# Kernel tuning notes

Measured on AMD Instinct MI355X. Metric: run time of the kernel, lower is better.

## Reference

```python
import jax, jax.numpy as jnp
import numpy as np

K = 8                   # num_RQS_bins
MIN_BW = 1e-6; MIN_BH = 1e-6; MIN_D = 1e-6
TAIL = 12.0             # tail_bound for 'linear' tails
# binary masks for num_inputs=4: kept (conditioning) dims and transformed dims per layer
MASK_IDX = [(0, 2), (1, 3), (0, 1), (2, 3)]
INV_IDX = [(1, 3), (0, 2), (2, 3), (0, 1)]


def _rqs_forward(x, uw, uh, ud):
    """Unconstrained rational-quadratic spline, forward (direct) pass.
    x: [B,F]; uw,uh: [B,F,K]; ud: [B,F,K-1]. Returns (y, logabsdet) each [B,F]."""
    const = float(np.log(np.exp(1.0 - MIN_D) - 1.0))
    ud = jnp.pad(ud, ((0, 0), (0, 0), (1, 1)), constant_values=const)  # [B,F,K+1]
    inside = (x >= -TAIL) & (x <= TAIL)
    xc = jnp.clip(x, -TAIL, TAIL)

    widths = MIN_BW + (1.0 - MIN_BW * K) * jax.nn.softmax(uw, -1)
    cumw = jnp.pad(jnp.cumsum(widths, -1), ((0, 0), (0, 0), (1, 0)))
    cumw = 2.0 * TAIL * cumw - TAIL
    cumw = cumw.at[..., 0].set(-TAIL).at[..., -1].set(TAIL)
    widths = cumw[..., 1:] - cumw[..., :-1]

    heights = MIN_BH + (1.0 - MIN_BH * K) * jax.nn.softmax(uh, -1)
    cumh = jnp.pad(jnp.cumsum(heights, -1), ((0, 0), (0, 0), (1, 0)))
    cumh = 2.0 * TAIL * cumh - TAIL
    cumh = cumh.at[..., 0].set(-TAIL).at[..., -1].set(TAIL)
    heights = cumh[..., 1:] - cumh[..., :-1]

    derivs = MIN_D + jax.nn.softplus(ud)  # [B,F,K+1]

    # searchsorted over bin edges (forward mode uses cumwidths)
    idx = jnp.clip(jnp.sum((xc[..., None] >= cumw).astype(jnp.int32), -1) - 1, 0, K - 1)
    g = lambda t: jnp.take_along_axis(t, idx[..., None], axis=-1)[..., 0]
    in_cw, in_w = g(cumw), g(widths)
    in_ch, in_h = g(cumh), g(heights)
    delta = in_h / in_w
    d_k, d_k1 = g(derivs), g(derivs[..., 1:])

    theta = (xc - in_cw) / in_w
    tomt = theta * (1.0 - theta)
    num = in_h * (delta * theta ** 2 + d_k * tomt)
    den = delta + (d_k + d_k1 - 2.0 * delta) * tomt
    y = in_ch + num / den
    dnum = delta ** 2 * (d_k1 * theta ** 2 + 2.0 * delta * tomt + d_k * (1.0 - theta) ** 2)
    lad = jnp.log(dnum) - 2.0 * jnp.log(den)

    return jnp.where(inside, y, x), jnp.where(inside, lad, 0.0)


def setup_inputs() -> dict:
    key = jax.random.key(0)
    ks = jax.random.split(key, 5)
    B, H = 262144, 128
    OM = 3 * K - 1  # 23 params per transformed dim
    inputs = jax.random.normal(ks[0], (B, 4), jnp.float32)
    cond_inputs = jax.random.uniform(ks[1], (B, 1), jnp.float32)
    W1 = jax.random.normal(ks[2], (4, H, 3), jnp.float32) / np.sqrt(3.0)
    b1 = jnp.zeros((4, H), jnp.float32)
    W2 = jax.random.normal(ks[3], (4, H, H), jnp.float32) / np.sqrt(float(H))
    b2 = jnp.zeros((4, H), jnp.float32)
    W3 = jax.random.normal(ks[4], (4, 2 * OM, H), jnp.float32) / np.sqrt(float(H))
    b3 = jnp.zeros((4, 2 * OM), jnp.float32)
    return {"inputs": inputs, "cond_inputs": cond_inputs,
            "W1": W1, "b1": b1, "W2": W2, "b2": b2, "W3": W3, "b3": b3}


def reference(inputs, cond_inputs, W1, b1, W2, b2, W3, b3):
    B = inputs.shape[0]
    x = inputs
    logdets = jnp.zeros((B, 1), dtype=inputs.dtype)
    for l in range(4):  # fixed small number of coupling layers
        midx = list(MASK_IDX[l]); iidx = list(INV_IDX[l])
        m_in = jnp.concatenate([x[:, midx], cond_inputs], -1)  # [B,3]
        h = jax.nn.relu(m_in @ W1[l].T + b1[l])
        h = jax.nn.relu(h @ W2[l].T + b2[l])
        params = h @ W3[l].T + b3[l]  # [B, F*(3K-1)]
        F = len(iidx)
        tp = jnp.swapaxes(params.reshape(B, 3 * K - 1, F), 1, 2)  # [B,F,3K-1]
        y, lad = _rqs_forward(x[:, iidx], tp[..., :K], tp[..., K:2 * K], tp[..., 2 * K:])
        x = x.at[:, iidx].set(y)
        logdets = logdets + jnp.sum(lad, -1, keepdims=True)
    return x, logdets
```

## Files before the change

kernel.cpp:

```cpp
#include <hip/hip_runtime.h>

#define TAILB 12.0f
#define INV2048 4.8828125e-4f

typedef _Float16 half8 __attribute__((ext_vector_type(8)));
typedef _Float16 half4 __attribute__((ext_vector_type(4)));
typedef __fp16 fp16x2 __attribute__((ext_vector_type(2)));
typedef __attribute__((ext_vector_type(4))) float f32x4;

#define MFMAH __builtin_amdgcn_mfma_f32_16x16x32_f16

#define WAVE_SYNC() do {                                  \
    __builtin_amdgcn_sched_barrier(0);                    \
    asm volatile("s_waitcnt lgkmcnt(0)" ::: "memory");    \
    __builtin_amdgcn_sched_barrier(0);                    \
} while (0)

__device__ __forceinline__ float softplus_f(float z) {
    return (z > 15.f) ? z : __logf(1.f + __expf(z));
}

__device__ __forceinline__ void split2h(float v, _Float16& o0, _Float16& o1) {
    _Float16 h0 = (_Float16)v;
    float r1 = v - (float)h0;
    o0 = h0;
    o1 = (_Float16)(r1 * 2048.0f);
}

__device__ __forceinline__ void split4_pk(const float* v, half4& p0, half4& p1) {
    fp16x2 lo = __builtin_amdgcn_cvt_pkrtz(v[0], v[1]);
    fp16x2 hi = __builtin_amdgcn_cvt_pkrtz(v[2], v[3]);
    float r0 = (v[0] - (float)lo.x) * 2048.f;
    float r1 = (v[1] - (float)lo.y) * 2048.f;
    float r2 = (v[2] - (float)hi.x) * 2048.f;
    float r3 = (v[3] - (float)hi.y) * 2048.f;
    fp16x2 rlo = __builtin_amdgcn_cvt_pkrtz(r0, r1);
    fp16x2 rhi = __builtin_amdgcn_cvt_pkrtz(r2, r3);
    p0 = (half4){(_Float16)lo.x, (_Float16)lo.y, (_Float16)hi.x, (_Float16)hi.y};
    p1 = (half4){(_Float16)rlo.x, (_Float16)rlo.y, (_Float16)rhi.x, (_Float16)rhi.y};
}

__global__ __launch_bounds__(256)
void prep_v16(const float* __restrict__ W1, const float* __restrict__ b1,
              const float* __restrict__ W2, const float* __restrict__ W3,
              _Float16* __restrict__ W2F, _Float16* __restrict__ W3F,
              float4* __restrict__ w1p)
{
    int id = blockIdx.x * 256 + threadIdx.x;
    if (id < 65536) {
        int j = id & 7, ln = (id >> 3) & 63, tile = id >> 9;
        int cs = tile & 3, t = (tile >> 2) & 1, wv = (tile >> 3) & 3, l = tile >> 5;
        int n = 32 * wv + 16 * t + (ln & 15);
        int k = 32 * cs + 8 * (ln >> 4) + j;
        _Float16 a, b;
        split2h(W2[l * 16384 + n * 128 + k], a, b);
        W2F[(tile * 2 + 0) * 512 + ln * 8 + j] = a;
        W2F[(tile * 2 + 1) * 512 + ln * 8 + j] = b;
    } else if (id < 90112) {
        int t2 = id - 65536;
        int j = t2 & 7, ln = (t2 >> 3) & 63, tile3 = t2 >> 9;
        int cs = tile3 & 3, q = tile3 >> 2;
        int wv = q % 3, l = q / 3;
        int p = 16 * wv + (ln & 15);
        int n = 32 * cs + 8 * (ln >> 4) + j;
        float v = (p < 46) ? W3[l * 5888 + p * 128 + n] : 0.f;
        _Float16 a, b;
        split2h(v, a, b);
        W3F[(tile3 * 2 + 0) * 512 + ln * 8 + j] = a;
        W3F[(tile3 * 2 + 1) * 512 + ln * 8 + j] = b;
    } else if (id < 90624) {
        int t = id - 90112;
        int l = t >> 7, k = t & 127;
        float4 v;
        v.x = W1[l * 384 + k * 3 + 0];
        v.y = W1[l * 384 + k * 3 + 1];
        v.z = W1[l * 384 + k * 3 + 2];
        v.w = b1[l * 128 + k];
        w1p[t] = v;
    }
}

__global__ __launch_bounds__(64, 3)
void rqs_v16(const float* __restrict__ inp, const float* __restrict__ cond,
             const _Float16* __restrict__ W2F, const _Float16* __restrict__ W3F,
             const float4* __restrict__ w1p,
             const float* __restrict__ b2, const float* __restrict__ b3,
             float* __restrict__ out, int B)
{
    __shared__ __align__(16) char P[8192];
    __shared__ float xbuf[32][5];

    char* plw = P;
    const char* pl = P;

    const int ln   = threadIdx.x;
    const int base = blockIdx.x * 32;
    const int sm   = ln & 15;
    const int qd   = ln >> 4;
    const int s1   = ln & 31;
    const int hi   = ln >> 5;

    int rdK[2][2];
    #pragma unroll
    for (int st = 0; st < 2; ++st)
        #pragma unroll
        for (int csl = 0; csl < 2; ++csl) {
            int row = 16 * st + sm;
            rdK[st][csl] = row * 128 + (((4 * csl + qd) ^ (row & 7)) << 4);
        }

    if (ln < 32) {
        float4 xi = reinterpret_cast<const float4*>(inp)[base + ln];
        xbuf[ln][0] = xi.x; xbuf[ln][1] = xi.y;
        xbuf[ln][2] = xi.z; xbuf[ln][3] = xi.w;
        xbuf[ln][4] = cond[base + ln];
    }
    float ladreg = 0.f;
    WAVE_SYNC();

    #pragma unroll 1
    for (int l = 0; l < 4; ++l) {
        int mi0, mi1, ii0, ii1;
        switch (l) {
            case 0:  mi0 = 0; mi1 = 2; ii0 = 1; ii1 = 3; break;
            case 1:  mi0 = 1; mi1 = 3; ii0 = 0; ii1 = 2; break;
            case 2:  mi0 = 0; mi1 = 1; ii0 = 2; ii1 = 3; break;
            default: mi0 = 2; mi1 = 3; ii0 = 0; ii1 = 1; break;
        }

        half8 bf[2][4][2];
        {
            float m0 = xbuf[s1][mi0], m1 = xbuf[s1][mi1], cc = xbuf[s1][4];
            const float4* w1l = w1p + l * 128;
            #pragma unroll
            for (int kh = 0; kh < 2; ++kh) {
                #pragma unroll
                for (int j4 = 0; j4 < 4; ++j4) {
                    int gl = 4 * hi + j4;
                    int g  = 8 * kh + gl;
                    float v[8];
                    #pragma unroll
                    for (int r = 0; r < 8; ++r) {
                        float4 w4 = w1l[g * 8 + r];
                        v[r] = fmaxf(fmaf(w4.x, m0, fmaf(w4.y, m1, fmaf(w4.z, cc, w4.w))), 0.f);
                    }
                    half4 a0, a1, b0h, b1h;
                    split4_pk(v, a0, a1);
                    split4_pk(v + 4, b0h, b1h);
                    half8 p0 = {a0.x, a0.y, a0.z, a0.w, b0h.x, b0h.y, b0h.z, b0h.w};
                    half8 p1 = {a1.x, a1.y, a1.z, a1.w, b1h.x, b1h.y, b1h.z, b1h.w};
                    char* wp = plw + s1 * 128 + ((gl ^ (s1 & 7)) << 4);
                    *(half8*)(wp)        = p0;
                    *(half8*)(wp + 4096) = p1;
                }
                WAVE_SYNC();
                #pragma unroll
                for (int st = 0; st < 2; ++st)
                    #pragma unroll
                    for (int csl = 0; csl < 2; ++csl) {
                        bf[st][2 * kh + csl][0] = *(const half8*)(pl + rdK[st][csl]);
                        bf[st][2 * kh + csl][1] = *(const half8*)(pl + rdK[st][csl] + 4096);
                    }
                WAVE_SYNC();
            }
        }

        half8 bf3[2][4][2];
        const half8* W2F8 = (const half8*)W2F;
        #pragma unroll
        for (int ntg = 0; ntg < 2; ++ntg) {
            #pragma unroll 1
            for (int ntl = 0; ntl < 4; ++ntl) {
                int nt = 4 * ntg + ntl;
                f32x4 accA[2], accB[2];
                float4 bias = *(const float4*)(b2 + l * 128 + nt * 16 + 4 * qd);
                #pragma unroll
                for (int st = 0; st < 2; ++st) {
                    accA[st] = (f32x4){bias.x, bias.y, bias.z, bias.w};
                    accB[st] = (f32x4){0.f, 0.f, 0.f, 0.f};
                }
                #pragma unroll
                for (int cs = 0; cs < 4; ++cs) {
                    int tile = l * 8 + nt;
                    half8 A0 = W2F8[((tile * 4 + cs) * 2 + 0) * 64 + ln];
                    half8 A1 = W2F8[((tile * 4 + cs) * 2 + 1) * 64 + ln];
                    #pragma unroll
                    for (int st = 0; st < 2; ++st) {
                        accA[st] = MFMAH(A0, bf[st][cs][0], accA[st], 0, 0, 0);
                        accB[st] = MFMAH(A0, bf[st][cs][1], accB[st], 0, 0, 0);
                        accB[st] = MFMAH(A1, bf[st][cs][0], accB[st], 0, 0, 0);
                    }
                }
                #pragma unroll
                for (int st = 0; st < 2; ++st) {
                    float v[4];
                    #pragma unroll
                    for (int r = 0; r < 4; ++r)
                        v[r] = fmaxf(fmaf(INV2048, accB[st][r], accA[st][r]), 0.f);
                    half4 p0, p1;
                    split4_pk(v, p0, p1);
                    int row = 16 * st + sm;
                    int gl  = 2 * ntl + (qd >> 1);
                    char* wp = plw + row * 128 + ((gl ^ (row & 7)) << 4) + ((qd & 1) << 3);
                    *(half4*)(wp)        = p0;
                    *(half4*)(wp + 4096) = p1;
                }
            }
            WAVE_SYNC();
            #pragma unroll
            for (int st = 0; st < 2; ++st)
                #pragma unroll
                for (int csl = 0; csl < 2; ++csl) {
                    bf3[st][2 * ntg + csl][0] = *(const half8*)(pl + rdK[st][csl]);
                    bf3[st][2 * ntg + csl][1] = *(const half8*)(pl + rdK[st][csl] + 4096);
                }
            WAVE_SYNC();
        }

        const half8* W3F8 = (const half8*)W3F;
        #pragma unroll 1
        for (int pt = 0; pt < 3; ++pt) {
            f32x4 a3A[2], a3B[2];
            #pragma unroll
            for (int st = 0; st < 2; ++st) {
                a3A[st] = (f32x4){0.f, 0.f, 0.f, 0.f};
                a3B[st] = (f32x4){0.f, 0.f, 0.f, 0.f};
            }
            #pragma unroll
            for (int cs = 0; cs < 4; ++cs) {
                int q = (l * 3 + pt) * 4 + cs;
                half8 A0 = W3F8[(q * 2 + 0) * 64 + ln];
                half8 A1 = W3F8[(q * 2 + 1) * 64 + ln];
                #pragma unroll
                for (int st = 0; st < 2; ++st) {
                    a3A[st] = MFMAH(A0, bf3[st][cs][0], a3A[st], 0, 0, 0);
                    a3B[st] = MFMAH(A0, bf3[st][cs][1], a3B[st], 0, 0, 0);
                    a3B[st] = MFMAH(A1, bf3[st][cs][0], a3B[st], 0, 0, 0);
                }
            }
            #pragma unroll
            for (int st = 0; st < 2; ++st) {
                float4 pv;
                pv.x = fmaf(INV2048, a3B[st][0], a3A[st][0]);
                pv.y = fmaf(INV2048, a3B[st][1], a3A[st][1]);
                pv.z = fmaf(INV2048, a3B[st][2], a3A[st][2]);
                pv.w = fmaf(INV2048, a3B[st][3], a3A[st][3]);
                *(float4*)(plw + (16 * st + sm) * 208 + (16 * pt + 4 * qd) * 4) = pv;
            }
        }
        WAVE_SYNC();

        {
            const float* b3l = b3 + l * 46;
            const float4* prow = (const float4*)(pl + s1 * 208);
            float pr[23];
            #pragma unroll
            for (int i = 0; i < 12; ++i) {
                float4 q = prow[i];
                pr[2 * i] = (hi ? q.y : q.x) + b3l[4 * i + hi];
                if (2 * i + 1 < 23)
                    pr[2 * i + 1] = (hi ? q.w : q.z) + b3l[4 * i + 2 + hi];
            }

            float xin = xbuf[s1][hi == 0 ? ii0 : ii1];

            float d[9];
            d[0] = 1.f; d[8] = 1.f;
            #pragma unroll
            for (int k = 1; k < 8; ++k) d[k] = 1e-6f + softplus_f(pr[16 + k - 1]);

            bool inside = (xin >= -TAILB) && (xin <= TAILB);
            float xc = fminf(fmaxf(xin, -TAILB), TAILB);

            float mw = pr[0], mh = pr[8];
            #pragma unroll
            for (int k = 1; k < 8; ++k) { mw = fmaxf(mw, pr[k]); mh = fmaxf(mh, pr[8 + k]); }
            float ew[8], eh[8], swm = 0.f, shm = 0.f;
            #pragma unroll
            for (int k = 0; k < 8; ++k) {
                ew[k] = __expf(pr[k] - mw);     swm += ew[k];
                eh[k] = __expf(pr[8 + k] - mh); shm += eh[k];
            }
            const float c1 = 1.f - 8e-6f;
            float isw = __fdividef(c1, swm), ish = __fdividef(c1, shm);

            float cum_w = 0.f, cum_h = 0.f;
            float cwk = -TAILB, chk = -TAILB;
            float s_cw = -TAILB, s_w = 2.f * TAILB, s_ch = -TAILB, s_h = 2.f * TAILB;
            float s_d0 = 1.f, s_d1 = d[1];
            #pragma unroll
            for (int k = 0; k < 8; ++k) {
                cum_w += fmaf(ew[k], isw, 1e-6f);
                cum_h += fmaf(eh[k], ish, 1e-6f);
                float cwn = (k == 7) ? TAILB : fmaf(2.f * TAILB, cum_w, -TAILB);
                float chn = (k == 7) ? TAILB : fmaf(2.f * TAILB, cum_h, -TAILB);
                bool ge = (xc >= cwk);
                s_cw = ge ? cwk : s_cw;  s_w = ge ? (cwn - cwk) : s_w;
                s_ch = ge ? chk : s_ch;  s_h = ge ? (chn - chk) : s_h;
                s_d0 = ge ? d[k] : s_d0; s_d1 = ge ? d[k + 1] : s_d1;
                cwk = cwn; chk = chn;
            }

            float rw    = __fdividef(1.f, s_w);
            float th    = (xc - s_cw) * rw;
            float delta = s_h * rw;
            float omt   = 1.f - th;
            float tomt  = th * omt;
            float num   = s_h * fmaf(delta, th * th, s_d0 * tomt);
            float den   = fmaf(s_d0 + s_d1 - 2.f * delta, tomt, delta);
            float y     = s_ch + __fdividef(num, den);
            float dnum  = delta * delta * (s_d1 * th * th + 2.f * delta * tomt + s_d0 * omt * omt);
            float lad   = __logf(dnum) - 2.f * __logf(den);

            xbuf[s1][hi == 0 ? ii0 : ii1] = inside ? y : xin;
            ladreg += inside ? lad : 0.f;
        }
        WAVE_SYNC();
    }

    float lsum = ladreg + __shfl(ladreg, (ln + 32) & 63, 64);
    if (ln < 32) {
        float4 xo;
        xo.x = xbuf[ln][0]; xo.y = xbuf[ln][1];
        xo.z = xbuf[ln][2]; xo.w = xbuf[ln][3];
        reinterpret_cast<float4*>(out)[base + ln] = xo;
        out[(size_t)B * 4 + base + ln] = lsum;
    }
}

extern "C" void kernel_launch(void* const* d_in, const int* in_sizes, int n_in,
                              void* d_out, int out_size, void* d_ws, size_t ws_size,
                              hipStream_t stream) {
    const float* inp  = (const float*)d_in[0];
    const float* cond = (const float*)d_in[1];
    const float* W1   = (const float*)d_in[2];
    const float* b1   = (const float*)d_in[3];
    const float* W2   = (const float*)d_in[4];
    const float* b2   = (const float*)d_in[5];
    const float* W3   = (const float*)d_in[6];
    const float* b3   = (const float*)d_in[7];
    float* out = (float*)d_out;
    int B = in_sizes[0] / 4;

    char* ws = (char*)d_ws;
    _Float16* W2F = (_Float16*)(ws);
    _Float16* W3F = (_Float16*)(ws + 262144);
    float4*   w1p = (float4*)(ws + 360448);

    hipLaunchKernelGGL(prep_v16, dim3(354), dim3(256), 0, stream,
                       W1, b1, W2, W3, W2F, W3F, w1p);
    hipLaunchKernelGGL(rqs_v16, dim3(B / 32), dim3(64), 0, stream,
                       inp, cond, W2F, W3F, w1p, b2, b3, out, B);
}
```

Baseline: 252.1 us.

## Pack two waves per block and shrink LDS staging to 32-column chunks

Each block now runs two independent waves, each handling 32 rows with its own smaller LDS staging area. Activations are staged in quarter-width chunks (64-byte rows with a new XOR swizzle) rather than half-width chunks. This cuts LDS per wave and raises the launch-bounds occupancy hint, so more waves can stay resident to hide latency. The price is more staging rounds and wave syncs per layer, plus register pressure from the tighter occupancy target.

```diff
diff --git a/kernel.cpp b/kernel.cpp
--- a/kernel.cpp
+++ b/kernel.cpp
@@ -41,7 +41,7 @@
 }
 
 __global__ __launch_bounds__(256)
-void prep_v16(const float* __restrict__ W1, const float* __restrict__ b1,
+void prep_v17(const float* __restrict__ W1, const float* __restrict__ b1,
               const float* __restrict__ W2, const float* __restrict__ W3,
               _Float16* __restrict__ W2F, _Float16* __restrict__ W3F,
               float4* __restrict__ w1p)
@@ -80,40 +80,39 @@
     }
 }
 
-__global__ __launch_bounds__(64, 3)
-void rqs_v16(const float* __restrict__ inp, const float* __restrict__ cond,
+__global__ __launch_bounds__(128, 5)
+void rqs_v17(const float* __restrict__ inp, const float* __restrict__ cond,
              const _Float16* __restrict__ W2F, const _Float16* __restrict__ W3F,
              const float4* __restrict__ w1p,
              const float* __restrict__ b2, const float* __restrict__ b3,
              float* __restrict__ out, int B)
 {
-    __shared__ __align__(16) char P[8192];
-    __shared__ float xbuf[32][5];
-
-    char* plw = P;
-    const char* pl = P;
-
-    const int ln   = threadIdx.x;
-    const int base = blockIdx.x * 32;
+    __shared__ __align__(16) char P[2][6656];
+    __shared__ float xbuf[2][32][5];
+
+    const int w  = threadIdx.x >> 6;
+    const int ln = threadIdx.x & 63;
+    char* plw = P[w];
+    const char* pl = plw;
+    float (*xb)[5] = xbuf[w];
+
+    const int base = blockIdx.x * 64 + w * 32;
     const int sm   = ln & 15;
     const int qd   = ln >> 4;
     const int s1   = ln & 31;
     const int hi   = ln >> 5;
-
-    int rdK[2][2];
+    const int usw  = (s1 >> 1) & 3;
+
+    int rdQ[2];
     #pragma unroll
     for (int st = 0; st < 2; ++st)
-        #pragma unroll
-        for (int csl = 0; csl < 2; ++csl) {
-            int row = 16 * st + sm;
-            rdK[st][csl] = row * 128 + (((4 * csl + qd) ^ (row & 7)) << 4);
-        }
+        rdQ[st] = (16 * st + sm) * 64 + ((qd ^ ((sm >> 1) & 3)) << 4);
 
     if (ln < 32) {
         float4 xi = reinterpret_cast<const float4*>(inp)[base + ln];
-        xbuf[ln][0] = xi.x; xbuf[ln][1] = xi.y;
-        xbuf[ln][2] = xi.z; xbuf[ln][3] = xi.w;
-        xbuf[ln][4] = cond[base + ln];
+        xb[ln][0] = xi.x; xb[ln][1] = xi.y;
+        xb[ln][2] = xi.z; xb[ln][3] = xi.w;
+        xb[ln][4] = cond[base + ln];
     }
     float ladreg = 0.f;
     WAVE_SYNC();
@@ -130,14 +129,13 @@
 
         half8 bf[2][4][2];
         {
-            float m0 = xbuf[s1][mi0], m1 = xbuf[s1][mi1], cc = xbuf[s1][4];
+            float m0 = xb[s1][mi0], m1 = xb[s1][mi1], cc = xb[s1][4];
             const float4* w1l = w1p + l * 128;
             #pragma unroll
-            for (int kh = 0; kh < 2; ++kh) {
-                #pragma unroll
-                for (int j4 = 0; j4 < 4; ++j4) {
-                    int gl = 4 * hi + j4;
-                    int g  = 8 * kh + gl;
+            for (int q = 0; q < 4; ++q) {
+                #pragma unroll
+                for (int gi = 0; gi < 2; ++gi) {
+                    int g = 4 * q + 2 * hi + gi;
                     float v[8];
                     #pragma unroll
                     for (int r = 0; r < 8; ++r) {
@@ -149,29 +147,28 @@
                     split4_pk(v + 4, b0h, b1h);
                     half8 p0 = {a0.x, a0.y, a0.z, a0.w, b0h.x, b0h.y, b0h.z, b0h.w};
                     half8 p1 = {a1.x, a1.y, a1.z, a1.w, b1h.x, b1h.y, b1h.z, b1h.w};
-                    char* wp = plw + s1 * 128 + ((gl ^ (s1 & 7)) << 4);
+                    int sl = (2 * hi + gi) ^ usw;
+                    char* wp = plw + s1 * 64 + (sl << 4);
                     *(half8*)(wp)        = p0;
-                    *(half8*)(wp + 4096) = p1;
+                    *(half8*)(wp + 2048) = p1;
                 }
                 WAVE_SYNC();
                 #pragma unroll
-                for (int st = 0; st < 2; ++st)
-                    #pragma unroll
-                    for (int csl = 0; csl < 2; ++csl) {
-                        bf[st][2 * kh + csl][0] = *(const half8*)(pl + rdK[st][csl]);
-                        bf[st][2 * kh + csl][1] = *(const half8*)(pl + rdK[st][csl] + 4096);
-                    }
+                for (int st = 0; st < 2; ++st) {
+                    bf[st][q][0] = *(const half8*)(pl + rdQ[st]);
+                    bf[st][q][1] = *(const half8*)(pl + rdQ[st] + 2048);
+                }
                 WAVE_SYNC();
             }
         }
 
         half8 bf3[2][4][2];
         const half8* W2F8 = (const half8*)W2F;
-        #pragma unroll
-        for (int ntg = 0; ntg < 2; ++ntg) {
-            #pragma unroll 1
-            for (int ntl = 0; ntl < 4; ++ntl) {
-                int nt = 4 * ntg + ntl;
+        #pragma unroll 1
+        for (int q = 0; q < 4; ++q) {
+            #pragma unroll
+            for (int ntl = 0; ntl < 2; ++ntl) {
+                int nt = 2 * q + ntl;
                 f32x4 accA[2], accB[2];
                 float4 bias = *(const float4*)(b2 + l * 128 + nt * 16 + 4 * qd);
                 #pragma unroll
@@ -200,20 +197,18 @@
                     half4 p0, p1;
                     split4_pk(v, p0, p1);
                     int row = 16 * st + sm;
-                    int gl  = 2 * ntl + (qd >> 1);
-                    char* wp = plw + row * 128 + ((gl ^ (row & 7)) << 4) + ((qd & 1) << 3);
+                    int sl  = (2 * ntl + (qd >> 1)) ^ ((sm >> 1) & 3);
+                    char* wp = plw + row * 64 + (sl << 4) + ((qd & 1) << 3);
                     *(half4*)(wp)        = p0;
-                    *(half4*)(wp + 4096) = p1;
+                    *(half4*)(wp + 2048) = p1;
                 }
             }
             WAVE_SYNC();
             #pragma unroll
-            for (int st = 0; st < 2; ++st)
-                #pragma unroll
-                for (int csl = 0; csl < 2; ++csl) {
-                    bf3[st][2 * ntg + csl][0] = *(const half8*)(pl + rdK[st][csl]);
-                    bf3[st][2 * ntg + csl][1] = *(const half8*)(pl + rdK[st][csl] + 4096);
-                }
+            for (int st = 0; st < 2; ++st) {
+                bf3[st][q][0] = *(const half8*)(pl + rdQ[st]);
+                bf3[st][q][1] = *(const half8*)(pl + rdQ[st] + 2048);
+            }
             WAVE_SYNC();
         }
 
@@ -262,7 +257,7 @@
                     pr[2 * i + 1] = (hi ? q.w : q.z) + b3l[4 * i + 2 + hi];
             }
 
-            float xin = xbuf[s1][hi == 0 ? ii0 : ii1];
+            float xin = xb[s1][hi == 0 ? ii0 : ii1];
 
             float d[9];
             d[0] = 1.f; d[8] = 1.f;
@@ -312,7 +307,7 @@
             float dnum  = delta * delta * (s_d1 * th * th + 2.f * delta * tomt + s_d0 * omt * omt);
             float lad   = __logf(dnum) - 2.f * __logf(den);
 
-            xbuf[s1][hi == 0 ? ii0 : ii1] = inside ? y : xin;
+            xb[s1][hi == 0 ? ii0 : ii1] = inside ? y : xin;
             ladreg += inside ? lad : 0.f;
         }
         WAVE_SYNC();
@@ -321,8 +316,8 @@
     float lsum = ladreg + __shfl(ladreg, (ln + 32) & 63, 64);
     if (ln < 32) {
         float4 xo;
-        xo.x = xbuf[ln][0]; xo.y = xbuf[ln][1];
-        xo.z = xbuf[ln][2]; xo.w = xbuf[ln][3];
+        xo.x = xb[ln][0]; xo.y = xb[ln][1];
+        xo.z = xb[ln][2]; xo.w = xb[ln][3];
         reinterpret_cast<float4*>(out)[base + ln] = xo;
         out[(size_t)B * 4 + base + ln] = lsum;
     }
@@ -347,8 +342,8 @@
     _Float16* W3F = (_Float16*)(ws + 262144);
     float4*   w1p = (float4*)(ws + 360448);
 
-    hipLaunchKernelGGL(prep_v16, dim3(354), dim3(256), 0, stream,
+    hipLaunchKernelGGL(prep_v17, dim3(354), dim3(256), 0, stream,
                        W1, b1, W2, W3, W2F, W3F, w1p);
-    hipLaunchKernelGGL(rqs_v16, dim3(B / 32), dim3(64), 0, stream,
+    hipLaunchKernelGGL(rqs_v17, dim3(B / 64), dim3(128), 0, stream,
                        inp, cond, W2F, W3F, w1p, b2, b3, out, B);
 }
```

After: 783.3 us. 211% more time.

## Build layer-1 MFMA operands in registers and stage layer-2 output in larger LDS

Applied to the files above, without the earlier changes.

Layer-1 activations are now computed straight into the MFMA B-operand register layout: each lane evaluates its own rows and k-range, so the LDS round trip and its two wave syncs per half are gone. Layer-2 results are written once into a doubled 16 KB LDS buffer with a new swizzle, and layer-3 reads its B operands from LDS inside the MFMA loop instead of holding bf3 in registers. The launch-bounds occupancy hint is dropped and the layer-3 pt loop is fully unrolled, with its results buffered before they are written out. This trades duplicated layer-1 FMAs and more LDS per block for fewer syncs and lower register pressure.

```diff
diff --git a/kernel.cpp b/kernel.cpp
--- a/kernel.cpp
+++ b/kernel.cpp
@@ -41,7 +41,7 @@
 }
 
 __global__ __launch_bounds__(256)
-void prep_v16(const float* __restrict__ W1, const float* __restrict__ b1,
+void prep_v20(const float* __restrict__ W1, const float* __restrict__ b1,
               const float* __restrict__ W2, const float* __restrict__ W3,
               _Float16* __restrict__ W2F, _Float16* __restrict__ W3F,
               float4* __restrict__ w1p)
@@ -80,14 +80,14 @@
     }
 }
 
-__global__ __launch_bounds__(64, 3)
-void rqs_v16(const float* __restrict__ inp, const float* __restrict__ cond,
+__global__ __launch_bounds__(64)
+void rqs_v20(const float* __restrict__ inp, const float* __restrict__ cond,
              const _Float16* __restrict__ W2F, const _Float16* __restrict__ W3F,
              const float4* __restrict__ w1p,
              const float* __restrict__ b2, const float* __restrict__ b3,
              float* __restrict__ out, int B)
 {
-    __shared__ __align__(16) char P[8192];
+    __shared__ __align__(16) char P[16384];
     __shared__ float xbuf[32][5];
 
     char* plw = P;
@@ -100,14 +100,12 @@
     const int s1   = ln & 31;
     const int hi   = ln >> 5;
 
-    int rdK[2][2];
+    int rdG3[2][4];
     #pragma unroll
     for (int st = 0; st < 2; ++st)
         #pragma unroll
-        for (int csl = 0; csl < 2; ++csl) {
-            int row = 16 * st + sm;
-            rdK[st][csl] = row * 128 + (((4 * csl + qd) ^ (row & 7)) << 4);
-        }
+        for (int cs = 0; cs < 4; ++cs)
+            rdG3[st][cs] = (16 * st + sm) * 256 + (((4 * cs + qd) ^ sm) << 4);
 
     if (ln < 32) {
         float4 xi = reinterpret_cast<const float4*>(inp)[base + ln];
@@ -130,95 +128,76 @@
 
         half8 bf[2][4][2];
         {
-            float m0 = xbuf[s1][mi0], m1 = xbuf[s1][mi1], cc = xbuf[s1][4];
+            float m0[2], m1[2], cc2[2];
+            #pragma unroll
+            for (int st = 0; st < 2; ++st) {
+                m0[st]  = xbuf[16 * st + sm][mi0];
+                m1[st]  = xbuf[16 * st + sm][mi1];
+                cc2[st] = xbuf[16 * st + sm][4];
+            }
             const float4* w1l = w1p + l * 128;
             #pragma unroll
-            for (int kh = 0; kh < 2; ++kh) {
+            for (int cs = 0; cs < 4; ++cs) {
+                float v0[8], v1[8];
                 #pragma unroll
-                for (int j4 = 0; j4 < 4; ++j4) {
-                    int gl = 4 * hi + j4;
-                    int g  = 8 * kh + gl;
-                    float v[8];
-                    #pragma unroll
-                    for (int r = 0; r < 8; ++r) {
-                        float4 w4 = w1l[g * 8 + r];
-                        v[r] = fmaxf(fmaf(w4.x, m0, fmaf(w4.y, m1, fmaf(w4.z, cc, w4.w))), 0.f);
-                    }
-                    half4 a0, a1, b0h, b1h;
-                    split4_pk(v, a0, a1);
-                    split4_pk(v + 4, b0h, b1h);
-                    half8 p0 = {a0.x, a0.y, a0.z, a0.w, b0h.x, b0h.y, b0h.z, b0h.w};
-                    half8 p1 = {a1.x, a1.y, a1.z, a1.w, b1h.x, b1h.y, b1h.z, b1h.w};
-                    char* wp = plw + s1 * 128 + ((gl ^ (s1 & 7)) << 4);
-                    *(half8*)(wp)        = p0;
-                    *(half8*)(wp + 4096) = p1;
+                for (int j = 0; j < 8; ++j) {
+                    float4 w4 = w1l[32 * cs + 8 * qd + j];
+                    v0[j] = fmaxf(fmaf(w4.x, m0[0], fmaf(w4.y, m1[0], fmaf(w4.z, cc2[0], w4.w))), 0.f);
+                    v1[j] = fmaxf(fmaf(w4.x, m0[1], fmaf(w4.y, m1[1], fmaf(w4.z, cc2[1], w4.w))), 0.f);
                 }
-                WAVE_SYNC();
-                #pragma unroll
-                for (int st = 0; st < 2; ++st)
-                    #pragma unroll
-                    for (int csl = 0; csl < 2; ++csl) {
-                        bf[st][2 * kh + csl][0] = *(const half8*)(pl + rdK[st][csl]);
-                        bf[st][2 * kh + csl][1] = *(const half8*)(pl + rdK[st][csl] + 4096);
-                    }
-                WAVE_SYNC();
-            }
-        }
-
-        half8 bf3[2][4][2];
+                half4 a0, a1, b0h, b1h;
+                split4_pk(v0, a0, a1);
+                split4_pk(v0 + 4, b0h, b1h);
+                bf[0][cs][0] = (half8){a0.x, a0.y, a0.z, a0.w, b0h.x, b0h.y, b0h.z, b0h.w};
+                bf[0][cs][1] = (half8){a1.x, a1.y, a1.z, a1.w, b1h.x, b1h.y, b1h.z, b1h.w};
+                split4_pk(v1, a0, a1);
+                split4_pk(v1 + 4, b0h, b1h);
+                bf[1][cs][0] = (half8){a0.x, a0.y, a0.z, a0.w, b0h.x, b0h.y, b0h.z, b0h.w};
+                bf[1][cs][1] = (half8){a1.x, a1.y, a1.z, a1.w, b1h.x, b1h.y, b1h.z, b1h.w};
+            }
+        }
+
         const half8* W2F8 = (const half8*)W2F;
-        #pragma unroll
-        for (int ntg = 0; ntg < 2; ++ntg) {
-            #pragma unroll 1
-            for (int ntl = 0; ntl < 4; ++ntl) {
-                int nt = 4 * ntg + ntl;
-                f32x4 accA[2], accB[2];
-                float4 bias = *(const float4*)(b2 + l * 128 + nt * 16 + 4 * qd);
+        #pragma unroll 2
+        for (int nt = 0; nt < 8; ++nt) {
+            f32x4 accA[2], accB[2];
+            float4 bias = *(const float4*)(b2 + l * 128 + nt * 16 + 4 * qd);
+            #pragma unroll
+            for (int st = 0; st < 2; ++st) {
+                accA[st] = (f32x4){bias.x, bias.y, bias.z, bias.w};
+                accB[st] = (f32x4){0.f, 0.f, 0.f, 0.f};
+            }
+            #pragma unroll
+            for (int cs = 0; cs < 4; ++cs) {
+                int tile = l * 8 + nt;
+                half8 A0 = W2F8[((tile * 4 + cs) * 2 + 0) * 64 + ln];
+                half8 A1 = W2F8[((tile * 4 + cs) * 2 + 1) * 64 + ln];
                 #pragma unroll
                 for (int st = 0; st < 2; ++st) {
-                    accA[st] = (f32x4){bias.x, bias.y, bias.z, bias.w};
-                    accB[st] = (f32x4){0.f, 0.f, 0.f, 0.f};
+                    accA[st] = MFMAH(A0, bf[st][cs][0], accA[st], 0, 0, 0);
+                    accB[st] = MFMAH(A0, bf[st][cs][1], accB[st], 0, 0, 0);
+                    accB[st] = MFMAH(A1, bf[st][cs][0], accB[st], 0, 0, 0);
                 }
+            }
+            #pragma unroll
+            for (int st = 0; st < 2; ++st) {
+                float v[4];
                 #pragma unroll
-                for (int cs = 0; cs < 4; ++cs) {
-                    int tile = l * 8 + nt;
-                    half8 A0 = W2F8[((tile * 4 + cs) * 2 + 0) * 64 + ln];
-                    half8 A1 = W2F8[((tile * 4 + cs) * 2 + 1) * 64 + ln];
-                    #pragma unroll
-                    for (int st = 0; st < 2; ++st) {
-                        accA[st] = MFMAH(A0, bf[st][cs][0], accA[st], 0, 0, 0);
-                        accB[st] = MFMAH(A0, bf[st][cs][1], accB[st], 0, 0, 0);
-                        accB[st] = MFMAH(A1, bf[st][cs][0], accB[st], 0, 0, 0);
-                    }
-                }
-                #pragma unroll
-                for (int st = 0; st < 2; ++st) {
-                    float v[4];
-                    #pragma unroll
-                    for (int r = 0; r < 4; ++r)
-                        v[r] = fmaxf(fmaf(INV2048, accB[st][r], accA[st][r]), 0.f);
-                    half4 p0, p1;
-                    split4_pk(v, p0, p1);
-                    int row = 16 * st + sm;
-                    int gl  = 2 * ntl + (qd >> 1);
-                    char* wp = plw + row * 128 + ((gl ^ (row & 7)) << 4) + ((qd & 1) << 3);
-                    *(half4*)(wp)        = p0;
-                    *(half4*)(wp + 4096) = p1;
-                }
-            }
-            WAVE_SYNC();
-            #pragma unroll
-            for (int st = 0; st < 2; ++st)
-                #pragma unroll
-                for (int csl = 0; csl < 2; ++csl) {
-                    bf3[st][2 * ntg + csl][0] = *(const half8*)(pl + rdK[st][csl]);
-                    bf3[st][2 * ntg + csl][1] = *(const half8*)(pl + rdK[st][csl] + 4096);
-                }
-            WAVE_SYNC();
-        }
+                for (int r = 0; r < 4; ++r)
+                    v[r] = fmaxf(fmaf(INV2048, accB[st][r], accA[st][r]), 0.f);
+                half4 p0, p1;
+                split4_pk(v, p0, p1);
+                int row = 16 * st + sm;
+                char* wp = plw + row * 256 + (((2 * nt + (qd >> 1)) ^ sm) << 4) + ((qd & 1) << 3);
+                *(half4*)(wp)        = p0;
+                *(half4*)(wp + 8192) = p1;
+            }
+        }
+        WAVE_SYNC();
 
         const half8* W3F8 = (const half8*)W3F;
-        #pragma unroll 1
+        f32x4 pvr[3][2];
+        #pragma unroll
         for (int pt = 0; pt < 3; ++pt) {
             f32x4 a3A[2], a3B[2];
             #pragma unroll
@@ -233,21 +212,28 @@
                 half8 A1 = W3F8[(q * 2 + 1) * 64 + ln];
                 #pragma unroll
                 for (int st = 0; st < 2; ++st) {
-                    a3A[st] = MFMAH(A0, bf3[st][cs][0], a3A[st], 0, 0, 0);
-                    a3B[st] = MFMAH(A0, bf3[st][cs][1], a3B[st], 0, 0, 0);
-                    a3B[st] = MFMAH(A1, bf3[st][cs][0], a3B[st], 0, 0, 0);
+                    half8 b0 = *(const half8*)(pl + rdG3[st][cs]);
+                    half8 b1 = *(const half8*)(pl + rdG3[st][cs] + 8192);
+                    a3A[st] = MFMAH(A0, b0, a3A[st], 0, 0, 0);
+                    a3B[st] = MFMAH(A0, b1, a3B[st], 0, 0, 0);
+                    a3B[st] = MFMAH(A1, b0, a3B[st], 0, 0, 0);
                 }
             }
             #pragma unroll
             for (int st = 0; st < 2; ++st) {
-                float4 pv;
-                pv.x = fmaf(INV2048, a3B[st][0], a3A[st][0]);
-                pv.y = fmaf(INV2048, a3B[st][1], a3A[st][1]);
-                pv.z = fmaf(INV2048, a3B[st][2], a3A[st][2]);
-                pv.w = fmaf(INV2048, a3B[st][3], a3A[st][3]);
+                pvr[pt][st][0] = fmaf(INV2048, a3B[st][0], a3A[st][0]);
+                pvr[pt][st][1] = fmaf(INV2048, a3B[st][1], a3A[st][1]);
+                pvr[pt][st][2] = fmaf(INV2048, a3B[st][2], a3A[st][2]);
+                pvr[pt][st][3] = fmaf(INV2048, a3B[st][3], a3A[st][3]);
+            }
+        }
+        #pragma unroll
+        for (int pt = 0; pt < 3; ++pt)
+            #pragma unroll
+            for (int st = 0; st < 2; ++st) {
+                float4 pv = {pvr[pt][st][0], pvr[pt][st][1], pvr[pt][st][2], pvr[pt][st][3]};
                 *(float4*)(plw + (16 * st + sm) * 208 + (16 * pt + 4 * qd) * 4) = pv;
             }
-        }
         WAVE_SYNC();
 
         {
@@ -347,8 +333,8 @@
     _Float16* W3F = (_Float16*)(ws + 262144);
     float4*   w1p = (float4*)(ws + 360448);
 
-    hipLaunchKernelGGL(prep_v16, dim3(354), dim3(256), 0, stream,
+    hipLaunchKernelGGL(prep_v20, dim3(354), dim3(256), 0, stream,
                        W1, b1, W2, W3, W2F, W3F, w1p);
-    hipLaunchKernelGGL(rqs_v16, dim3(B / 32), dim3(64), 0, stream,
+    hipLaunchKernelGGL(rqs_v20, dim3(B / 32), dim3(64), 0, stream,
                        inp, cond, W2F, W3F, w1p, b2, b3, out, B);
 }
```

After: 281.0 us. 11.5% more time.
